# Optimization experiments

Measured on AMD Instinct MI355X. Metric: run time of the kernel, lower is better.

Reference implementation:

```python
import jax, jax.numpy as jnp
import numpy as np

N_SEARCH, B, C, H, W = 10, 32, 768, 24, 24
HT, WT = 8, 8
HEADS, POOL = 12, 4


def _G(t):
    # Integral of the bilinear triangle kernel: G(t) = int_{-1}^{t} max(0,1-|s|) ds
    tc = jnp.clip(t, -1.0, 1.0)
    return 0.5 + tc * (1.0 - 0.5 * jnp.abs(tc))


def prroi_pool(feats, rois, pool):
    # feats: [R,C,H,W], rois: [R,4] pixel coords (x0,y0,x1,y1); exact PrRoIPool2D
    R, C_, H_, W_ = feats.shape
    x0, y0, x1, y1 = rois[:, 0], rois[:, 1], rois[:, 2], rois[:, 3]
    bw = (x1 - x0) / pool
    bh = (y1 - y0) / pool
    p = jnp.arange(pool, dtype=feats.dtype)
    ex0 = x0[:, None] + p[None, :] * bw[:, None]   # [R,pool]
    ex1 = ex0 + bw[:, None]
    ey0 = y0[:, None] + p[None, :] * bh[:, None]
    ey1 = ey0 + bh[:, None]
    ix = jnp.arange(W_, dtype=feats.dtype)
    iy = jnp.arange(H_, dtype=feats.dtype)
    wx = _G(ex1[:, :, None] - ix) - _G(ex0[:, :, None] - ix)  # [R,pool,W]
    wy = _G(ey1[:, :, None] - iy) - _G(ey0[:, :, None] - iy)  # [R,pool,H]
    area = jnp.maximum(bw * bh, 1e-8)[:, None, None, None]
    return jnp.einsum('rph,rqw,rchw->rcpq', wy, wx, feats) / area  # [R,C,pool,pool]


def layernorm(x, g, b, eps=1e-5):
    m = jnp.mean(x, -1, keepdims=True)
    v = jnp.mean((x - m) ** 2, -1, keepdims=True)
    return (x - m) * jax.lax.rsqrt(v + eps) * g + b


def setup_inputs():
    key = jax.random.key(0)
    ks = jax.random.split(key, 24)
    search_feats = jax.random.normal(ks[0], (N_SEARCH, B, C, H, W), jnp.float32)
    template_feat = jax.random.normal(ks[1], (N_SEARCH, B, C, HT, WT), jnp.float32)
    u = jax.random.uniform(ks[2], (N_SEARCH, B, 4), jnp.float32)
    x0 = 0.05 + 0.4 * u[..., 0]
    y0 = 0.05 + 0.4 * u[..., 1]
    x1 = x0 + 0.15 + 0.3 * u[..., 2]
    y1 = y0 + 0.15 + 0.3 * u[..., 3]
    search_boxes = jnp.stack([x0, y0, x1, y1], -1)  # normalized, x1>x0, y1>y0
    s = 0.02
    d = {
        'search_feats': search_feats,
        'template_feat': template_feat,
        'search_boxes': search_boxes,
        'score_token': s * jax.random.normal(ks[3], (1, 1, C), jnp.float32),
        'ln1_g': jnp.ones((C,), jnp.float32), 'ln1_b': jnp.zeros((C,), jnp.float32),
        'Wq': s * jax.random.normal(ks[4], (2, C, C), jnp.float32), 'bq': jnp.zeros((2, C), jnp.float32),
        'Wk': s * jax.random.normal(ks[5], (2, C, C), jnp.float32), 'bk': jnp.zeros((2, C), jnp.float32),
        'Wv': s * jax.random.normal(ks[6], (2, C, C), jnp.float32), 'bv': jnp.zeros((2, C), jnp.float32),
        'Wo': s * jax.random.normal(ks[7], (2, C, C), jnp.float32), 'bo': jnp.zeros((2, C), jnp.float32),
        'ln2_g': jnp.ones((2, C), jnp.float32), 'ln2_b': jnp.zeros((2, C), jnp.float32),
        'Wmix': s * jax.random.normal(ks[8], (2, N_SEARCH, N_SEARCH), jnp.float32),
        'bmix': jnp.zeros((2, N_SEARCH), jnp.float32),
        'W1': s * jax.random.normal(ks[9], (C, C), jnp.float32), 'b1': jnp.zeros((C,), jnp.float32),
        'W2': s * jax.random.normal(ks[10], (C, C), jnp.float32), 'b2': jnp.zeros((C,), jnp.float32),
        'W3': s * jax.random.normal(ks[11], (C, 1), jnp.float32), 'b3': jnp.zeros((1,), jnp.float32),
    }
    return d


def reference(search_feats, template_feat, search_boxes, score_token, ln1_g, ln1_b,
              Wq, bq, Wk, bk, Wv, bv, Wo, bo, ln2_g, ln2_b, Wmix, bmix,
              W1, b1, W2, b2, W3, b3):
    N, b, c, h, w = search_feats.shape
    heads, pool = HEADS, POOL
    dh = c // heads
    scale = c ** (-0.5)  # note: full hidden_dim scale, as in original

    boxes = (search_boxes * w).reshape(-1, 4)              # [N*b,4] pixel coords
    feats = search_feats.reshape(-1, c, h, w)              # [N*b,c,h,w]
    pooled = prroi_pool(feats, boxes, pool)                # [N*b,c,pool,pool]
    # 'b c h w -> b (h w) c' then split N
    sbf = pooled.reshape(N, b, c, pool * pool).transpose(0, 1, 3, 2)  # [N,b,16,c]
    tmpl = template_feat.reshape(N, b, c, -1).transpose(0, 1, 3, 2)   # [N,b,64,c]

    x = jnp.broadcast_to(score_token, (N, b, 1, c))
    x = layernorm(x, ln1_g, ln1_b)
    kv = [sbf, tmpl]
    for i in range(2):
        q = x @ Wq[i] + bq[i]                              # [N,b,1,c]
        k = kv[i] @ Wk[i] + bk[i]                          # [N,b,T,c]
        v = kv[i] @ Wv[i] + bv[i]
        T = k.shape[2]
        qh = q.reshape(N, b, 1, heads, dh).transpose(0, 1, 3, 2, 4)   # [N,b,H,1,d]
        kh = k.reshape(N, b, T, heads, dh).transpose(0, 1, 3, 2, 4)   # [N,b,H,T,d]
        vh = v.reshape(N, b, T, heads, dh).transpose(0, 1, 3, 2, 4)
        attn = jax.nn.softmax(jnp.einsum('nbhld,nbhtd->nbhlt', qh, kh) * scale, -1)
        o = jnp.einsum('nbhlt,nbhtd->nbhld', attn, vh)
        o = o.transpose(0, 1, 3, 2, 4).reshape(N, b, 1, c)
        o = layernorm(o @ Wo[i] + bo[i], ln2_g[i], ln2_b[i])
        # time-mix across the N frames: [N,b,1,c] -> [b,c,N] -> linear -> [N,b,1,c]
        t = o[:, :, 0, :].transpose(1, 2, 0)               # [b,c,N]
        t = t @ Wmix[i] + bmix[i]
        x = t.transpose(2, 0, 1)[:, :, None, :]            # [N,b,1,c]

    hdd = jax.nn.relu(x @ W1 + b1)
    hdd = jax.nn.relu(hdd @ W2 + b2)
    return hdd @ W3 + b3                                   # [N,b,1,1]
```

## Files before the change

### kernel.cpp

```cpp
#include <hip/hip_runtime.h>
#include <cstdint>
#include <cstddef>

namespace {

constexpr float kScale = 0.03608439182435161f;
constexpr float kEps   = 1e-5f;

constexpr size_t OFF_QK0T = 0;
constexpr size_t OFF_QBK0 = 9216;
constexpr size_t OFF_S    = 16384;
constexpr size_t OFF_QK1  = OFF_S   + 2949120;
constexpr size_t OFF_O    = OFF_QK1 + 2949120;
constexpr size_t OFF_U    = OFF_O   + 245760;
constexpr size_t OFF_X    = OFF_U   + 245760;
constexpr size_t OFF_QF1  = OFF_X   + 245760;
constexpr size_t OFF_H1   = OFF_QF1 + 245760;
constexpr size_t OFF_H2   = OFF_H1  + 245760;
constexpr size_t OFF_WF   = OFF_H2  + 245760;

constexpr size_t WF_MAT_SHORTS = 1179648;

typedef short short8v __attribute__((ext_vector_type(8)));
typedef float float4v __attribute__((ext_vector_type(4)));

union BP  { int4 i4; short8v s8; };
union S4P { int2 i2; short s[4]; };

__device__ __forceinline__ void splitBf(float a, short &h, short &l){
    unsigned u = __float_as_uint(a);
    h = (short)(u >> 16);
    float r = a - __uint_as_float(u & 0xFFFF0000u);
    l = (short)(__float_as_uint(r) >> 16);
}

__device__ __forceinline__ float Gf(float t){
    float tc = fminf(fmaxf(t, -1.f), 1.f);
    return 0.5f + tc * (1.f - 0.5f * fabsf(tc));
}

__device__ __forceinline__ float blockReduce256(float v, float* red){
    #pragma unroll
    for (int off = 1; off < 64; off <<= 1) v += __shfl_xor(v, off);
    __syncthreads();
    if ((threadIdx.x & 63) == 0) red[threadIdx.x >> 6] = v;
    __syncthreads();
    return red[0] + red[1] + red[2] + red[3];
}

__global__ __launch_bounds__(256) void k_wprep(
        const float* __restrict__ w0, const float* __restrict__ w1,
        const float* __restrict__ w2, const float* __restrict__ w3,
        const float* __restrict__ w4, const float* __restrict__ w5,
        const float* __restrict__ w6, short* __restrict__ WF){
    const float* Wsel[7] = {w0,w1,w2,w3,w4,w5,w6};
    const float* W = Wsel[blockIdx.y];
    const int unit = blockIdx.x * 4 + (threadIdx.x >> 6);
    const int l = threadIdx.x & 63;
    const int kt = unit / 48, nb = unit % 48;
    const int n = nb*16 + (l & 15);
    const int kb = kt*32 + ((l >> 4) << 2);
    S4P hi0, hi1, lo0, lo1;
    #pragma unroll
    for (int e = 0; e < 4; ++e){
        float a = W[(size_t)(kb + e) * 768 + n];
        splitBf(a, hi0.s[e], lo0.s[e]);
        float b = W[(size_t)(kb + 16 + e) * 768 + n];
        splitBf(b, hi1.s[e], lo1.s[e]);
    }
    size_t base = (size_t)blockIdx.y * WF_MAT_SHORTS + (size_t)unit * 1024 + (size_t)l * 8;
    *(int2*)(WF + base)            = hi0.i2;
    *(int2*)(WF + base + 4)        = hi1.i2;
    *(int2*)(WF + base + 512)      = lo0.i2;
    *(int2*)(WF + base + 512 + 4)  = lo1.i2;
}

template<int HG, int RELU>
__global__ __launch_bounds__(256) void k_mgemm(
        const float* __restrict__ A, const short* __restrict__ WFm,
        const float* __restrict__ bias, float* __restrict__ C){
    __shared__ short AF[2][2][2][64][8];
    const int h   = blockIdx.y;
    const int m0  = blockIdx.x * 32;
    const int tid = threadIdx.x;
    const int l   = tid & 63;
    const int w   = tid >> 6;
    const int wm  = w >> 1, wn = w & 1;

    const int srow = tid >> 3, sk4 = tid & 7;
    const int sfm  = srow >> 4;
    const int slane = (srow & 15) + 16 * (sk4 & 3);
    const int sebase = 4 * (sk4 >> 2);
    const float* aRow = HG ? (A + ((size_t)(m0 + srow) * 12 + h) * 768)
                           : (A + (size_t)(m0 + srow) * 768);

    const int nb0 = h * 4 + wn * 2;
    const short* WB = WFm + (size_t)nb0 * 1024 + (size_t)l * 8;

    float4v acc0 = {0.f,0.f,0.f,0.f};
    float4v acc1 = {0.f,0.f,0.f,0.f};

    {
        float4 a0 = *(const float4*)(aRow + sk4 * 4);
        S4P hi, lo;
        splitBf(a0.x, hi.s[0], lo.s[0]); splitBf(a0.y, hi.s[1], lo.s[1]);
        splitBf(a0.z, hi.s[2], lo.s[2]); splitBf(a0.w, hi.s[3], lo.s[3]);
        *(int2*)&AF[0][sfm][0][slane][sebase] = hi.i2;
        *(int2*)&AF[0][sfm][1][slane][sebase] = lo.i2;
    }
    BP bh0, bl0, bh1, bl1;
    bh0.i4 = *(const int4*)(WB);
    bl0.i4 = *(const int4*)(WB + 512);
    bh1.i4 = *(const int4*)(WB + 1024);
    bl1.i4 = *(const int4*)(WB + 1536);
    __syncthreads();

    #pragma unroll 1
    for (int kt = 0; kt < 24; ++kt){
        const int cur = kt & 1;
        const int ktn = (kt < 23) ? kt + 1 : 23;
        float4 aN = *(const float4*)(aRow + ktn * 32 + sk4 * 4);
        BP cbh0 = bh0, cbl0 = bl0, cbh1 = bh1, cbl1 = bl1;
        {
            const short* wb = WB + (size_t)ktn * 49152;
            bh0.i4 = *(const int4*)(wb);
            bl0.i4 = *(const int4*)(wb + 512);
            bh1.i4 = *(const int4*)(wb + 1024);
            bl1.i4 = *(const int4*)(wb + 1536);
        }
        short8v ah = *(short8v*)&AF[cur][wm][0][l][0];
        short8v al = *(short8v*)&AF[cur][wm][1][l][0];
        acc0 = __builtin_amdgcn_mfma_f32_16x16x32_bf16(ah, cbh0.s8, acc0, 0, 0, 0);
        acc0 = __builtin_amdgcn_mfma_f32_16x16x32_bf16(al, cbh0.s8, acc0, 0, 0, 0);
        acc0 = __builtin_amdgcn_mfma_f32_16x16x32_bf16(ah, cbl0.s8, acc0, 0, 0, 0);
        acc1 = __builtin_amdgcn_mfma_f32_16x16x32_bf16(ah, cbh1.s8, acc1, 0, 0, 0);
        acc1 = __builtin_amdgcn_mfma_f32_16x16x32_bf16(al, cbh1.s8, acc1, 0, 0, 0);
        acc1 = __builtin_amdgcn_mfma_f32_16x16x32_bf16(ah, cbl1.s8, acc1, 0, 0, 0);
        if (kt < 23){
            S4P hi, lo;
            splitBf(aN.x, hi.s[0], lo.s[0]); splitBf(aN.y, hi.s[1], lo.s[1]);
            splitBf(aN.z, hi.s[2], lo.s[2]); splitBf(aN.w, hi.s[3], lo.s[3]);
            *(int2*)&AF[cur ^ 1][sfm][0][slane][sebase] = hi.i2;
            *(int2*)&AF[cur ^ 1][sfm][1][slane][sebase] = lo.i2;
        }
        __syncthreads();
    }

    const int col0 = h * 64 + (wn * 2 + 0) * 16 + (l & 15);
    const int col1 = h * 64 + (wn * 2 + 1) * 16 + (l & 15);
    const float b0 = bias[col0], b1 = bias[col1];
    #pragma unroll
    for (int reg = 0; reg < 4; ++reg){
        int row = m0 + wm * 16 + ((l >> 4) << 2) + reg;
        float v0 = acc0[reg] + b0;
        float v1 = acc1[reg] + b1;
        if (RELU){ v0 = fmaxf(v0, 0.f); v1 = fmaxf(v1, 0.f); }
        C[(size_t)row * 768 + col0] = v0;
        C[(size_t)row * 768 + col1] = v1;
    }
}

__global__ __launch_bounds__(256) void k_prep(
        const float* __restrict__ token, const float* __restrict__ g1,
        const float* __restrict__ b1,    const float* __restrict__ Wq0,
        const float* __restrict__ bq0,   const float* __restrict__ Wk0,
        const float* __restrict__ bk0,
        float* __restrict__ qk0T, float* __restrict__ qbk0){
    __shared__ float x0l[768];
    __shared__ float red[8];
    __shared__ float qfp[4][64];
    __shared__ float qfl[64];
    __shared__ float Ws[64][68];
    const int h  = blockIdx.x / 12;
    const int ct = blockIdx.x % 12;
    const int tid = threadIdx.x;

    float v0 = token[tid], v1 = token[tid+256], v2 = token[tid+512];
    float s = blockReduce256(v0+v1+v2, red);
    float m = s * (1.f/768.f);
    float d0 = v0-m, d1 = v1-m, d2 = v2-m;
    float qv = blockReduce256(d0*d0+d1*d1+d2*d2, red);
    float rs = rsqrtf(qv*(1.f/768.f) + kEps);
    x0l[tid]     = d0*rs*g1[tid]     + b1[tid];
    x0l[tid+256] = d1*rs*g1[tid+256] + b1[tid+256];
    x0l[tid+512] = d2*rs*g1[tid+512] + b1[tid+512];
    __syncthreads();

    {
        int dl = tid & 63, part = tid >> 6;
        int d = h*64 + dl;
        float a = 0.f;
        for (int c = part*192; c < part*192 + 192; ++c)
            a += x0l[c] * Wq0[(size_t)c*768 + d];
        qfp[part][dl] = a;
    }
    __syncthreads();
    if (tid < 64){
        int d = h*64 + tid;
        qfl[tid] = qfp[0][tid]+qfp[1][tid]+qfp[2][tid]+qfp[3][tid] + bq0[d];
    }
    __syncthreads();
    if (ct == 0 && tid < 64){
        float v = qfl[tid] * bk0[h*64 + tid];
        #pragma unroll
        for (int off = 1; off < 64; off <<= 1) v += __shfl_xor(v, off);
        if (tid == 0) qbk0[h] = v;
    }
    #pragma unroll
    for (int i = 0; i < 4; ++i){
        int f = tid + i*256; int cl = f >> 4, dd = (f & 15)*4;
        float4 v = *(const float4*)(Wk0 + (size_t)(ct*64+cl)*768 + h*64 + dd);
        *(float4*)&Ws[cl][dd] = v;
    }
    __syncthreads();
    {
        int cl = tid >> 2, part = tid & 3;
        float a = 0.f;
        #pragma unroll
        for (int jj = 0; jj < 16; ++jj){
            int dd = part*16 + jj;
            a += Ws[cl][dd] * qfl[dd];
        }
        a += __shfl_xor(a, 1); a += __shfl_xor(a, 2);
        if (part == 0) qk0T[h*768 + ct*64 + cl] = a;
    }
}

__global__ __launch_bounds__(256) void k_pool(
        const float* __restrict__ feats, const float* __restrict__ boxes,
        const float* __restrict__ qk0T,  const float* __restrict__ qbk0g,
        float* __restrict__ s0){
    __shared__ float P2[16][776];
    __shared__ float wxp[24][4];
    __shared__ float wyp[24][4];
    __shared__ float logitsL[12][17];
    __shared__ float attnT[16][12];
    __shared__ int   rng[4];
    __shared__ float areaInvS;
    const int r = blockIdx.x, tid = threadIdx.x;

    float bx0 = boxes[r*4+0]*24.f, by0 = boxes[r*4+1]*24.f;
    float bx1 = boxes[r*4+2]*24.f, by1 = boxes[r*4+3]*24.f;
    float bw = (bx1-bx0)*0.25f, bh = (by1-by0)*0.25f;
    if (tid == 0){
        int hlo = (int)floorf(by0) - 1; if (hlo < 0) hlo = 0;
        int hhi = (int)floorf(by1) + 1; if (hhi > 23) hhi = 23;
        int wlo = (int)floorf(bx0) - 1; if (wlo < 0) wlo = 0;
        int whi = (int)floorf(bx1) + 1; if (whi > 23) whi = 23;
        rng[0] = hlo; rng[1] = hhi; rng[2] = wlo >> 2; rng[3] = whi >> 2;
        areaInvS = 1.f / fmaxf(bw*bh, 1e-8f);
    }
    if (tid < 24){
        int w = tid;
        #pragma unroll
        for (int q = 0; q < 4; ++q){
            float e0 = bx0 + q*bw, e1 = e0 + bw;
            wxp[w][q] = Gf(e1 - (float)w) - Gf(e0 - (float)w);
        }
    } else if (tid < 48){
        int hh = tid - 24;
        #pragma unroll
        for (int p = 0; p < 4; ++p){
            float e0 = by0 + p*bh, e1 = e0 + bh;
            wyp[hh][p] = Gf(e1 - (float)hh) - Gf(e0 - (float)hh);
        }
    }
    __syncthreads();
    const int hlo = rng[0], hhi = rng[1], w4lo = rng[2], w4hi = rng[3];
    const float aInv = areaInvS;
    const int j = tid & 7;
    const int cbase = tid >> 3;

    for (int cg = 0; cg < 24; ++cg){
        int c = cg*32 + cbase;
        const float* fb = feats + ((size_t)r*768 + c)*576;
        float acc[16];
        #pragma unroll
        for (int k = 0; k < 16; ++k) acc[k] = 0.f;
        for (int hh = hlo + j; hh <= hhi; hh += 8){
            const float* rowp = fb + hh*24;
            float z[4] = {0.f,0.f,0.f,0.f};
            for (int w4 = w4lo; w4 <= w4hi; ++w4){
                float4 xv = *(const float4*)(rowp + w4*4);
                float xa[4] = {xv.x, xv.y, xv.z, xv.w};
                #pragma unroll
                for (int k = 0; k < 4; ++k){
                    float4 wv = *(const float4*)&wxp[w4*4+k][0];
                    z[0] += wv.x*xa[k]; z[1] += wv.y*xa[k];
                    z[2] += wv.z*xa[k]; z[3] += wv.w*xa[k];
                }
            }
            float4 wyv = *(const float4*)&wyp[hh][0];
            float wya[4] = {wyv.x, wyv.y, wyv.z, wyv.w};
            #pragma unroll
            for (int p = 0; p < 4; ++p)
                #pragma unroll
                for (int q = 0; q < 4; ++q)
                    acc[p*4+q] += wya[p]*z[q];
        }
        #pragma unroll
        for (int k = 0; k < 16; ++k){
            acc[k] += __shfl_xor(acc[k], 1);
            acc[k] += __shfl_xor(acc[k], 2);
            acc[k] += __shfl_xor(acc[k], 4);
        }
        P2[j][c]   = acc[j]   * aInv;
        P2[j+8][c] = acc[j+8] * aInv;
    }
    __syncthreads();

    if (tid < 192){
        int h = tid >> 4, t = tid & 15;
        float a = qbk0g[h];
        const float* qrow = qk0T + h*768;
        #pragma unroll 4
        for (int c4 = 0; c4 < 192; ++c4){
            float4 qv = *(const float4*)(qrow + c4*4);
            float4 pv = *(const float4*)&P2[t][c4*4];
            a += qv.x*pv.x + qv.y*pv.y + qv.z*pv.z + qv.w*pv.w;
        }
        logitsL[h][t] = a * kScale;
    }
    __syncthreads();
    if (tid < 12){
        float mx = -1e30f;
        for (int t = 0; t < 16; ++t) mx = fmaxf(mx, logitsL[tid][t]);
        float ss = 0.f;
        for (int t = 0; t < 16; ++t){
            float e = expf(logitsL[tid][t] - mx);
            attnT[t][tid] = e; ss += e;
        }
        float rsn = 1.f/ss;
        for (int t = 0; t < 16; ++t) attnT[t][tid] *= rsn;
    }
    __syncthreads();
    #pragma unroll
    for (int s3 = 0; s3 < 3; ++s3){
        int c = tid + s3*256;
        float a12[12];
        #pragma unroll
        for (int h = 0; h < 12; ++h) a12[h] = 0.f;
        #pragma unroll
        for (int t = 0; t < 16; ++t){
            float x = P2[t][c];
            float4 a0 = *(const float4*)&attnT[t][0];
            float4 a1 = *(const float4*)&attnT[t][4];
            float4 a2 = *(const float4*)&attnT[t][8];
            a12[0] += a0.x*x; a12[1] += a0.y*x; a12[2]  += a0.z*x; a12[3]  += a0.w*x;
            a12[4] += a1.x*x; a12[5] += a1.y*x; a12[6]  += a1.z*x; a12[7]  += a1.w*x;
            a12[8] += a2.x*x; a12[9] += a2.y*x; a12[10] += a2.z*x; a12[11] += a2.w*x;
        }
        #pragma unroll
        for (int h = 0; h < 12; ++h)
            s0[((size_t)r*12 + h)*768 + c] = a12[h];
    }
}

__global__ __launch_bounds__(256) void k_qk1(
        const float* __restrict__ qf1, const float* __restrict__ Wk1,
        float* __restrict__ qk1){
    __shared__ float As[32][68];
    __shared__ float Bs[64][68];
    const int r0 = blockIdx.x * 32, h = blockIdx.y, c0 = blockIdx.z * 64;
    const int tid = threadIdx.x;
    #pragma unroll
    for (int i = 0; i < 2; ++i){
        int f = tid + i*256; int ml = f >> 4, kk = (f & 15)*4;
        *(float4*)&As[ml][kk] =
            *(const float4*)(qf1 + (size_t)(r0+ml)*768 + h*64 + kk);
    }
    #pragma unroll
    for (int i = 0; i < 4; ++i){
        int f = tid + i*256; int cl = f >> 4, dd = (f & 15)*4;
        float4 v = *(const float4*)(Wk1 + (size_t)(c0+cl)*768 + h*64 + dd);
        Bs[dd+0][cl] = v.x; Bs[dd+1][cl] = v.y;
        Bs[dd+2][cl] = v.z; Bs[dd+3][cl] = v.w;
    }
    __syncthreads();
    const int tn = tid & 15, tm = tid >> 4;
    float acc0[4] = {0.f,0.f,0.f,0.f};
    float acc1[4] = {0.f,0.f,0.f,0.f};
    #pragma unroll
    for (int k4 = 0; k4 < 16; ++k4){
        float4 av0 = *(const float4*)&As[tm*2+0][k4*4];
        float4 av1 = *(const float4*)&As[tm*2+1][k4*4];
        float a0a[4] = {av0.x, av0.y, av0.z, av0.w};
        float a1a[4] = {av1.x, av1.y, av1.z, av1.w};
        #pragma unroll
        for (int jj = 0; jj < 4; ++jj){
            float4 bv = *(const float4*)&Bs[k4*4+jj][tn*4];
            acc0[0] += a0a[jj]*bv.x; acc0[1] += a0a[jj]*bv.y;
            acc0[2] += a0a[jj]*bv.z; acc0[3] += a0a[jj]*bv.w;
            acc1[0] += a1a[jj]*bv.x; acc1[1] += a1a[jj]*bv.y;
            acc1[2] += a1a[jj]*bv.z; acc1[3] += a1a[jj]*bv.w;
        }
    }
    float4 o0; o0.x=acc0[0]; o0.y=acc0[1]; o0.z=acc0[2]; o0.w=acc0[3];
    float4 o1; o1.x=acc1[0]; o1.y=acc1[1]; o1.z=acc1[2]; o1.w=acc1[3];
    *(float4*)(qk1 + ((size_t)(r0+tm*2+0)*12 + h)*768 + c0 + tn*4) = o0;
    *(float4*)(qk1 + ((size_t)(r0+tm*2+1)*12 + h)*768 + c0 + tn*4) = o1;
}

__global__ __launch_bounds__(256) void k_attn1(
        const float* __restrict__ tmpl, const float* __restrict__ qf1,
        const float* __restrict__ bk1,  const float* __restrict__ qk1,
        float* __restrict__ s1){
    __shared__ float Tc[192][68];
    __shared__ float logitsT[64][13];
    __shared__ float attnH[12][64];
    __shared__ float qbk[12];
    const int r = blockIdx.x, tid = threadIdx.x;
    const float* tp = tmpl + (size_t)r*768*64;

    if (tid < 192){
        int h = tid >> 4, pp = tid & 15;
        float v = 0.f;
        #pragma unroll
        for (int jj = 0; jj < 4; ++jj){
            int d = h*64 + pp*4 + jj;
            v += bk1[d] * qf1[(size_t)r*768 + d];
        }
        v += __shfl_xor(v,1); v += __shfl_xor(v,2);
        v += __shfl_xor(v,4); v += __shfl_xor(v,8);
        if (pp == 0) qbk[h] = v;
    }
    __syncthreads();
    float lacc[3];
    #pragma unroll
    for (int s = 0; s < 3; ++s){
        int task = tid + s*256;
        lacc[s] = qbk[task >> 6];
    }
    for (int cb = 0; cb < 4; ++cb){
        #pragma unroll
        for (int i = 0; i < 12; ++i){
            int f = tid + i*256; int cl = f >> 4, t4 = (f & 15)*4;
            *(float4*)&Tc[cl][t4] =
                *(const float4*)(tp + (size_t)(cb*192 + cl)*64 + t4);
        }
        __syncthreads();
        #pragma unroll
        for (int s = 0; s < 3; ++s){
            int task = tid + s*256;
            int h = task >> 6, t = task & 63;
            const float* qrow = qk1 + ((size_t)r*12 + h)*768 + cb*192;
            float a = 0.f;
            #pragma unroll 4
            for (int c4 = 0; c4 < 48; ++c4){
                float4 qv = *(const float4*)(qrow + c4*4);
                a += qv.x*Tc[c4*4+0][t] + qv.y*Tc[c4*4+1][t]
                   + qv.z*Tc[c4*4+2][t] + qv.w*Tc[c4*4+3][t];
            }
            lacc[s] += a;
        }
        __syncthreads();
    }
    #pragma unroll
    for (int s = 0; s < 3; ++s){
        int task = tid + s*256;
        logitsT[task & 63][task >> 6] = lacc[s] * kScale;
    }
    __syncthreads();
    if (tid < 12){
        float mx = -1e30f;
        for (int t = 0; t < 64; ++t) mx = fmaxf(mx, logitsT[t][tid]);
        float ss = 0.f;
        for (int t = 0; t < 64; ++t){
            float e = expf(logitsT[t][tid] - mx);
            attnH[tid][t] = e; ss += e;
        }
        float rsn = 1.f/ss;
        for (int t = 0; t < 64; ++t) attnH[tid][t] *= rsn;
    }
    __syncthreads();
    for (int cb = 0; cb < 4; ++cb){
        #pragma unroll
        for (int i = 0; i < 12; ++i){
            int f = tid + i*256; int cl = f >> 4, t4 = (f & 15)*4;
            *(float4*)&Tc[cl][t4] =
                *(const float4*)(tp + (size_t)(cb*192 + cl)*64 + t4);
        }
        __syncthreads();
        if (tid < 192){
            float4 trow[16];
            #pragma unroll
            for (int t4 = 0; t4 < 16; ++t4)
                trow[t4] = *(const float4*)&Tc[tid][t4*4];
            int c = cb*192 + tid;
            #pragma unroll
            for (int h = 0; h < 12; ++h){
                float a = 0.f;
                #pragma unroll
                for (int t4 = 0; t4 < 16; ++t4){
                    float4 avv = *(const float4*)&attnH[h][t4*4];
                    float4 tv = trow[t4];
                    a += avv.x*tv.x + avv.y*tv.y + avv.z*tv.z + avv.w*tv.w;
                }
                s1[((size_t)r*12 + h)*768 + c] = a;
            }
        }
        __syncthreads();
    }
}

__global__ __launch_bounds__(256) void k_lnmix(
        const float* __restrict__ u, const float* __restrict__ g,
        const float* __restrict__ bta, const float* __restrict__ Wmix,
        const float* __restrict__ bmix, float* __restrict__ xout){
    __shared__ float lnl[10][768];
    __shared__ float red[8];
    __shared__ float wm[100];
    __shared__ float bm[10];
    const int b = blockIdx.x, tid = threadIdx.x;
    if (tid < 100) wm[tid] = Wmix[tid];
    if (tid < 10)  bm[tid] = bmix[tid];
    for (int n = 0; n < 10; ++n){
        const float* row = u + (size_t)(n*32 + b)*768;
        float v0 = row[tid], v1 = row[tid+256], v2 = row[tid+512];
        float s = blockReduce256(v0+v1+v2, red);
        float m = s * (1.f/768.f);
        float d0 = v0-m, d1 = v1-m, d2 = v2-m;
        float qv = blockReduce256(d0*d0+d1*d1+d2*d2, red);
        float rs = rsqrtf(qv*(1.f/768.f) + kEps);
        lnl[n][tid]     = d0*rs*g[tid]     + bta[tid];
        lnl[n][tid+256] = d1*rs*g[tid+256] + bta[tid+256];
        lnl[n][tid+512] = d2*rs*g[tid+512] + bta[tid+512];
    }
    __syncthreads();
    #pragma unroll
    for (int s3 = 0; s3 < 3; ++s3){
        int c = tid + s3*256;
        float col[10];
        #pragma unroll
        for (int n = 0; n < 10; ++n) col[n] = lnl[n][c];
        #pragma unroll
        for (int np = 0; np < 10; ++np){
            float a = bm[np];
            #pragma unroll
            for (int n = 0; n < 10; ++n) a += col[n]*wm[n*10+np];
            xout[(size_t)(np*32 + b)*768 + c] = a;
        }
    }
}

__global__ __launch_bounds__(256) void k_head(
        const float* __restrict__ h2v, const float* __restrict__ W3,
        const float* __restrict__ b3, float* __restrict__ out){
    __shared__ float red[8];
    const int r = blockIdx.x, tid = threadIdx.x;
    const float* row = h2v + (size_t)r*768;
    float a = row[tid]*W3[tid] + row[tid+256]*W3[tid+256] + row[tid+512]*W3[tid+512];
    a = blockReduce256(a, red);
    if (tid == 0) out[r] = a + b3[0];
}

}

extern "C" void kernel_launch(void* const* d_in, const int* in_sizes, int n_in,
                              void* d_out, int out_size, void* d_ws, size_t ws_size,
                              hipStream_t stream){
    const float* feats = (const float*)d_in[0];
    const float* tmpl  = (const float*)d_in[1];
    const float* boxes = (const float*)d_in[2];
    const float* token = (const float*)d_in[3];
    const float* ln1g  = (const float*)d_in[4];
    const float* ln1b  = (const float*)d_in[5];
    const float* Wq    = (const float*)d_in[6];
    const float* bq    = (const float*)d_in[7];
    const float* Wk    = (const float*)d_in[8];
    const float* bk    = (const float*)d_in[9];
    const float* Wv    = (const float*)d_in[10];
    const float* bv    = (const float*)d_in[11];
    const float* Wo    = (const float*)d_in[12];
    const float* bo    = (const float*)d_in[13];
    const float* ln2g  = (const float*)d_in[14];
    const float* ln2b  = (const float*)d_in[15];
    const float* Wmix  = (const float*)d_in[16];
    const float* bmix  = (const float*)d_in[17];
    const float* W1    = (const float*)d_in[18];
    const float* b1v   = (const float*)d_in[19];
    const float* W2    = (const float*)d_in[20];
    const float* b2v   = (const float*)d_in[21];
    const float* W3    = (const float*)d_in[22];
    const float* b3v   = (const float*)d_in[23];
    float* ws  = (float*)d_ws;
    float* out = (float*)d_out;

    float* qk0T = ws + OFF_QK0T;
    float* qbk0 = ws + OFF_QBK0;
    float* sbuf = ws + OFF_S;
    float* qk1  = ws + OFF_QK1;
    float* obuf = ws + OFF_O;
    float* ubuf = ws + OFF_U;
    float* xbuf = ws + OFF_X;
    float* qf1  = ws + OFF_QF1;
    float* h1b  = ws + OFF_H1;
    float* h2b  = ws + OFF_H2;
    short* wf   = (short*)(ws + OFF_WF);

    const size_t MO = 589824;
    short* wfv0 = wf + 0*WF_MAT_SHORTS;
    short* wfo0 = wf + 1*WF_MAT_SHORTS;
    short* wfq1 = wf + 2*WF_MAT_SHORTS;
    short* wfv1 = wf + 3*WF_MAT_SHORTS;
    short* wfo1 = wf + 4*WF_MAT_SHORTS;
    short* wf1  = wf + 5*WF_MAT_SHORTS;
    short* wf2  = wf + 6*WF_MAT_SHORTS;

    k_wprep<<<dim3(288,7), 256, 0, stream>>>(Wv, Wo, Wq + MO, Wv + MO, Wo + MO, W1, W2, wf);
    k_prep<<<144, 256, 0, stream>>>(token, ln1g, ln1b, Wq, bq, Wk, bk, qk0T, qbk0);
    k_pool<<<320, 256, 0, stream>>>(feats, boxes, qk0T, qbk0, sbuf);
    k_mgemm<1,0><<<dim3(10,12), 256, 0, stream>>>(sbuf, wfv0, bv, obuf);
    k_mgemm<0,0><<<dim3(10,12), 256, 0, stream>>>(obuf, wfo0, bo, ubuf);
    k_lnmix<<<32, 256, 0, stream>>>(ubuf, ln2g, ln2b, Wmix, bmix, xbuf);
    k_mgemm<0,0><<<dim3(10,12), 256, 0, stream>>>(xbuf, wfq1, bq + 768, qf1);
    k_qk1<<<dim3(10,12,12), 256, 0, stream>>>(qf1, Wk + MO, qk1);
    k_attn1<<<320, 256, 0, stream>>>(tmpl, qf1, bk + 768, qk1, sbuf);
    k_mgemm<1,0><<<dim3(10,12), 256, 0, stream>>>(sbuf, wfv1, bv + 768, obuf);
    k_mgemm<0,0><<<dim3(10,12), 256, 0, stream>>>(obuf, wfo1, bo + 768, ubuf);
    k_lnmix<<<32, 256, 0, stream>>>(ubuf, ln2g + 768, ln2b + 768, Wmix + 100, bmix + 10, xbuf);
    k_mgemm<0,1><<<dim3(10,12), 256, 0, stream>>>(xbuf, wf1, b1v, h1b);
    k_mgemm<0,1><<<dim3(10,12), 256, 0, stream>>>(h1b, wf2, b2v, h2b);
    k_head<<<320, 256, 0, stream>>>(h2b, W3, b3v, out);
}
```

Baseline: 424.6 us.

## Split pooling across channel blocks and halve GEMM row tile for more blocks

```diff
diff --git a/kernel.cpp b/kernel.cpp
--- a/kernel.cpp
+++ b/kernel.cpp
@@ -18,8 +18,8 @@
 constexpr size_t OFF_H1   = OFF_QF1 + 245760;
 constexpr size_t OFF_H2   = OFF_H1  + 245760;
 constexpr size_t OFF_WF   = OFF_H2  + 245760;
-
 constexpr size_t WF_MAT_SHORTS = 1179648;
+constexpr size_t OFF_P    = OFF_WF + (7*WF_MAT_SHORTS)/2;
 
 typedef short short8v __attribute__((ext_vector_type(8)));
 typedef float float4v __attribute__((ext_vector_type(4)));
@@ -79,84 +79,72 @@
 __global__ __launch_bounds__(256) void k_mgemm(
         const float* __restrict__ A, const short* __restrict__ WFm,
         const float* __restrict__ bias, float* __restrict__ C){
-    __shared__ short AF[2][2][2][64][8];
+    __shared__ short AF[2][2][64][8];
     const int h   = blockIdx.y;
-    const int m0  = blockIdx.x * 32;
+    const int m0  = blockIdx.x * 16;
     const int tid = threadIdx.x;
     const int l   = tid & 63;
     const int w   = tid >> 6;
-    const int wm  = w >> 1, wn = w & 1;
 
     const int srow = tid >> 3, sk4 = tid & 7;
-    const int sfm  = srow >> 4;
-    const int slane = (srow & 15) + 16 * (sk4 & 3);
+    const int slane = srow + 16 * (sk4 & 3);
     const int sebase = 4 * (sk4 >> 2);
     const float* aRow = HG ? (A + ((size_t)(m0 + srow) * 12 + h) * 768)
                            : (A + (size_t)(m0 + srow) * 768);
 
-    const int nb0 = h * 4 + wn * 2;
-    const short* WB = WFm + (size_t)nb0 * 1024 + (size_t)l * 8;
-
-    float4v acc0 = {0.f,0.f,0.f,0.f};
-    float4v acc1 = {0.f,0.f,0.f,0.f};
-
-    {
+    const int nb = h * 4 + w;
+    const short* WB = WFm + (size_t)nb * 1024 + (size_t)l * 8;
+
+    float4v acc = {0.f,0.f,0.f,0.f};
+
+    if (tid < 128){
         float4 a0 = *(const float4*)(aRow + sk4 * 4);
         S4P hi, lo;
         splitBf(a0.x, hi.s[0], lo.s[0]); splitBf(a0.y, hi.s[1], lo.s[1]);
         splitBf(a0.z, hi.s[2], lo.s[2]); splitBf(a0.w, hi.s[3], lo.s[3]);
-        *(int2*)&AF[0][sfm][0][slane][sebase] = hi.i2;
-        *(int2*)&AF[0][sfm][1][slane][sebase] = lo.i2;
-    }
-    BP bh0, bl0, bh1, bl1;
-    bh0.i4 = *(const int4*)(WB);
-    bl0.i4 = *(const int4*)(WB + 512);
-    bh1.i4 = *(const int4*)(WB + 1024);
-    bl1.i4 = *(const int4*)(WB + 1536);
+        *(int2*)&AF[0][0][slane][sebase] = hi.i2;
+        *(int2*)&AF[0][1][slane][sebase] = lo.i2;
+    }
+    BP bh, bl;
+    bh.i4 = *(const int4*)(WB);
+    bl.i4 = *(const int4*)(WB + 512);
     __syncthreads();
 
     #pragma unroll 1
     for (int kt = 0; kt < 24; ++kt){
         const int cur = kt & 1;
         const int ktn = (kt < 23) ? kt + 1 : 23;
-        float4 aN = *(const float4*)(aRow + ktn * 32 + sk4 * 4);
-        BP cbh0 = bh0, cbl0 = bl0, cbh1 = bh1, cbl1 = bl1;
+        float4 aN;
+        if (tid < 128) aN = *(const float4*)(aRow + ktn * 32 + sk4 * 4);
+        BP cbh = bh, cbl = bl;
         {
             const short* wb = WB + (size_t)ktn * 49152;
-            bh0.i4 = *(const int4*)(wb);
-            bl0.i4 = *(const int4*)(wb + 512);
-            bh1.i4 = *(const int4*)(wb + 1024);
-            bl1.i4 = *(const int4*)(wb + 1536);
-        }
-        short8v ah = *(short8v*)&AF[cur][wm][0][l][0];
-        short8v al = *(short8v*)&AF[cur][wm][1][l][0];
-        acc0 = __builtin_amdgcn_mfma_f32_16x16x32_bf16(ah, cbh0.s8, acc0, 0, 0, 0);
-        acc0 = __builtin_amdgcn_mfma_f32_16x16x32_bf16(al, cbh0.s8, acc0, 0, 0, 0);
-        acc0 = __builtin_amdgcn_mfma_f32_16x16x32_bf16(ah, cbl0.s8, acc0, 0, 0, 0);
-        acc1 = __builtin_amdgcn_mfma_f32_16x16x32_bf16(ah, cbh1.s8, acc1, 0, 0, 0);
-        acc1 = __builtin_amdgcn_mfma_f32_16x16x32_bf16(al, cbh1.s8, acc1, 0, 0, 0);
-        acc1 = __builtin_amdgcn_mfma_f32_16x16x32_bf16(ah, cbl1.s8, acc1, 0, 0, 0);
-        if (kt < 23){
+            bh.i4 = *(const int4*)(wb);
+            bl.i4 = *(const int4*)(wb + 512);
+        }
+        short8v ah = *(short8v*)&AF[cur][0][l][0];
+        short8v al = *(short8v*)&AF[cur][1][l][0];
+        acc = __builtin_amdgcn_mfma_f32_16x16x32_bf16(ah, cbh.s8, acc, 0, 0, 0);
+        acc = __builtin_amdgcn_mfma_f32_16x16x32_bf16(al, cbh.s8, acc, 0, 0, 0);
+        acc = __builtin_amdgcn_mfma_f32_16x16x32_bf16(ah, cbl.s8, acc, 0, 0, 0);
+        if (kt < 23 && tid < 128){
             S4P hi, lo;
             splitBf(aN.x, hi.s[0], lo.s[0]); splitBf(aN.y, hi.s[1], lo.s[1]);
             splitBf(aN.z, hi.s[2], lo.s[2]); splitBf(aN.w, hi.s[3], lo.s[3]);
-            *(int2*)&AF[cur ^ 1][sfm][0][slane][sebase] = hi.i2;
-            *(int2*)&AF[cur ^ 1][sfm][1][slane][sebase] = lo.i2;
+            *(int2*)&AF[cur ^ 1][0][slane][sebase] = hi.i2;
+            *(int2*)&AF[cur ^ 1][1][slane][sebase] = lo.i2;
         }
         __syncthreads();
     }
 
-    const int col0 = h * 64 + (wn * 2 + 0) * 16 + (l & 15);
-    const int col1 = h * 64 + (wn * 2 + 1) * 16 + (l & 15);
-    const float b0 = bias[col0], b1 = bias[col1];
+    const int col = h * 64 + w * 16 + (l & 15);
+    const float bb = bias[col];
     #pragma unroll
     for (int reg = 0; reg < 4; ++reg){
-        int row = m0 + wm * 16 + ((l >> 4) << 2) + reg;
-        float v0 = acc0[reg] + b0;
-        float v1 = acc1[reg] + b1;
-        if (RELU){ v0 = fmaxf(v0, 0.f); v1 = fmaxf(v1, 0.f); }
-        C[(size_t)row * 768 + col0] = v0;
-        C[(size_t)row * 768 + col1] = v1;
+        int row = m0 + ((l >> 4) << 2) + reg;
+        float v = acc[reg] + bb;
+        if (RELU) v = fmaxf(v, 0.f);
+        C[(size_t)row * 768 + col] = v;
     }
 }
 
@@ -226,18 +214,15 @@
     }
 }
 
-__global__ __launch_bounds__(256) void k_pool(
+__global__ __launch_bounds__(256) void k_pool2(
         const float* __restrict__ feats, const float* __restrict__ boxes,
-        const float* __restrict__ qk0T,  const float* __restrict__ qbk0g,
-        float* __restrict__ s0){
-    __shared__ float P2[16][776];
+        float* __restrict__ P){
+    __shared__ float Xs[32*580];
     __shared__ float wxp[24][4];
     __shared__ float wyp[24][4];
-    __shared__ float logitsL[12][17];
-    __shared__ float attnT[16][12];
-    __shared__ int   rng[4];
+    __shared__ int   rng[2];
     __shared__ float areaInvS;
-    const int r = blockIdx.x, tid = threadIdx.x;
+    const int r = blockIdx.x, cc = blockIdx.y * 32, tid = threadIdx.x;
 
     float bx0 = boxes[r*4+0]*24.f, by0 = boxes[r*4+1]*24.f;
     float bx1 = boxes[r*4+2]*24.f, by1 = boxes[r*4+3]*24.f;
@@ -245,9 +230,7 @@
     if (tid == 0){
         int hlo = (int)floorf(by0) - 1; if (hlo < 0) hlo = 0;
         int hhi = (int)floorf(by1) + 1; if (hhi > 23) hhi = 23;
-        int wlo = (int)floorf(bx0) - 1; if (wlo < 0) wlo = 0;
-        int whi = (int)floorf(bx1) + 1; if (whi > 23) whi = 23;
-        rng[0] = hlo; rng[1] = hhi; rng[2] = wlo >> 2; rng[3] = whi >> 2;
+        rng[0] = hlo; rng[1] = hhi - hlo + 1;
         areaInvS = 1.f / fmaxf(bw*bh, 1e-8f);
     }
     if (tid < 24){
@@ -266,46 +249,77 @@
         }
     }
     __syncthreads();
-    const int hlo = rng[0], hhi = rng[1], w4lo = rng[2], w4hi = rng[3];
+    const int hlo = rng[0], nr = rng[1];
     const float aInv = areaInvS;
+
+    const int nf4 = nr * 192;
+    for (int idx = tid; idx < nf4; idx += 256){
+        int ri  = idx / 192;
+        int rem = idx - ri * 192;
+        int cl  = rem / 6;
+        int w4  = rem - cl * 6;
+        float4 v = *(const float4*)(feats + ((size_t)(r*768 + cc + cl))*576
+                                    + (hlo + ri)*24 + w4*4);
+        *(float4*)&Xs[cl*580 + ri*24 + w4*4] = v;
+    }
+    __syncthreads();
+
     const int j = tid & 7;
-    const int cbase = tid >> 3;
-
-    for (int cg = 0; cg < 24; ++cg){
-        int c = cg*32 + cbase;
-        const float* fb = feats + ((size_t)r*768 + c)*576;
-        float acc[16];
-        #pragma unroll
-        for (int k = 0; k < 16; ++k) acc[k] = 0.f;
-        for (int hh = hlo + j; hh <= hhi; hh += 8){
-            const float* rowp = fb + hh*24;
-            float z[4] = {0.f,0.f,0.f,0.f};
-            for (int w4 = w4lo; w4 <= w4hi; ++w4){
-                float4 xv = *(const float4*)(rowp + w4*4);
-                float xa[4] = {xv.x, xv.y, xv.z, xv.w};
-                #pragma unroll
-                for (int k = 0; k < 4; ++k){
-                    float4 wv = *(const float4*)&wxp[w4*4+k][0];
-                    z[0] += wv.x*xa[k]; z[1] += wv.y*xa[k];
-                    z[2] += wv.z*xa[k]; z[3] += wv.w*xa[k];
-                }
+    const int cl = tid >> 3;
+    float acc[16];
+    #pragma unroll
+    for (int k = 0; k < 16; ++k) acc[k] = 0.f;
+    for (int ri = j; ri < nr; ri += 8){
+        const float* xr = &Xs[cl*580 + ri*24];
+        float z[4] = {0.f,0.f,0.f,0.f};
+        #pragma unroll
+        for (int w4 = 0; w4 < 6; ++w4){
+            float4 xv = *(const float4*)(xr + w4*4);
+            float xa[4] = {xv.x, xv.y, xv.z, xv.w};
+            #pragma unroll
+            for (int k = 0; k < 4; ++k){
+                float4 wv = *(const float4*)&wxp[w4*4+k][0];
+                z[0] += wv.x*xa[k]; z[1] += wv.y*xa[k];
+                z[2] += wv.z*xa[k]; z[3] += wv.w*xa[k];
             }
-            float4 wyv = *(const float4*)&wyp[hh][0];
-            float wya[4] = {wyv.x, wyv.y, wyv.z, wyv.w};
+        }
+        float4 wyv = *(const float4*)&wyp[hlo+ri][0];
+        float wya[4] = {wyv.x, wyv.y, wyv.z, wyv.w};
+        #pragma unroll
+        for (int p = 0; p < 4; ++p)
             #pragma unroll
-            for (int p = 0; p < 4; ++p)
-                #pragma unroll
-                for (int q = 0; q < 4; ++q)
-                    acc[p*4+q] += wya[p]*z[q];
-        }
-        #pragma unroll
-        for (int k = 0; k < 16; ++k){
-            acc[k] += __shfl_xor(acc[k], 1);
-            acc[k] += __shfl_xor(acc[k], 2);
-            acc[k] += __shfl_xor(acc[k], 4);
-        }
-        P2[j][c]   = acc[j]   * aInv;
-        P2[j+8][c] = acc[j+8] * aInv;
+            for (int q = 0; q < 4; ++q)
+                acc[p*4+q] += wya[p]*z[q];
+    }
+    #pragma unroll
+    for (int k = 0; k < 16; ++k){
+        acc[k] += __shfl_xor(acc[k], 1);
+        acc[k] += __shfl_xor(acc[k], 2);
+        acc[k] += __shfl_xor(acc[k], 4);
+    }
+    float o0 = acc[0], o1 = acc[8];
+    #pragma unroll
+    for (int k = 1; k < 8; ++k){
+        if (j == k){ o0 = acc[k]; o1 = acc[k+8]; }
+    }
+    P[((size_t)r*16 + j)*768 + cc + cl]     = o0 * aInv;
+    P[((size_t)r*16 + j + 8)*768 + cc + cl] = o1 * aInv;
+}
+
+__global__ __launch_bounds__(256) void k_attn0(
+        const float* __restrict__ P, const float* __restrict__ qk0T,
+        const float* __restrict__ qbk0g, float* __restrict__ s0){
+    __shared__ float P2[16][776];
+    __shared__ float logitsL[12][17];
+    __shared__ float attnT[16][12];
+    const int r = blockIdx.x, tid = threadIdx.x;
+
+    #pragma unroll
+    for (int i = 0; i < 12; ++i){
+        int f = tid + i*256;
+        int t = f / 192, c4 = f - t*192;
+        float4 v = *(const float4*)(P + ((size_t)r*16 + t)*768 + c4*4);
+        *(float4*)&P2[t][c4*4] = v;
     }
     __syncthreads();
 
@@ -597,6 +611,7 @@
     float* h1b  = ws + OFF_H1;
     float* h2b  = ws + OFF_H2;
     short* wf   = (short*)(ws + OFF_WF);
+    float* Pbuf = ws + OFF_P;
 
     const size_t MO = 589824;
     short* wfv0 = wf + 0*WF_MAT_SHORTS;
@@ -609,17 +624,18 @@
 
     k_wprep<<<dim3(288,7), 256, 0, stream>>>(Wv, Wo, Wq + MO, Wv + MO, Wo + MO, W1, W2, wf);
     k_prep<<<144, 256, 0, stream>>>(token, ln1g, ln1b, Wq, bq, Wk, bk, qk0T, qbk0);
-    k_pool<<<320, 256, 0, stream>>>(feats, boxes, qk0T, qbk0, sbuf);
-    k_mgemm<1,0><<<dim3(10,12), 256, 0, stream>>>(sbuf, wfv0, bv, obuf);
-    k_mgemm<0,0><<<dim3(10,12), 256, 0, stream>>>(obuf, wfo0, bo, ubuf);
+    k_pool2<<<dim3(320,24), 256, 0, stream>>>(feats, boxes, Pbuf);
+    k_attn0<<<320, 256, 0, stream>>>(Pbuf, qk0T, qbk0, sbuf);
+    k_mgemm<1,0><<<dim3(20,12), 256, 0, stream>>>(sbuf, wfv0, bv, obuf);
+    k_mgemm<0,0><<<dim3(20,12), 256, 0, stream>>>(obuf, wfo0, bo, ubuf);
     k_lnmix<<<32, 256, 0, stream>>>(ubuf, ln2g, ln2b, Wmix, bmix, xbuf);
-    k_mgemm<0,0><<<dim3(10,12), 256, 0, stream>>>(xbuf, wfq1, bq + 768, qf1);
+    k_mgemm<0,0><<<dim3(20,12), 256, 0, stream>>>(xbuf, wfq1, bq + 768, qf1);
     k_qk1<<<dim3(10,12,12), 256, 0, stream>>>(qf1, Wk + MO, qk1);
     k_attn1<<<320, 256, 0, stream>>>(tmpl, qf1, bk + 768, qk1, sbuf);
-    k_mgemm<1,0><<<dim3(10,12), 256, 0, stream>>>(sbuf, wfv1, bv + 768, obuf);
-    k_mgemm<0,0><<<dim3(10,12), 256, 0, stream>>>(obuf, wfo1, bo + 768, ubuf);
+    k_mgemm<1,0><<<dim3(20,12), 256, 0, stream>>>(sbuf, wfv1, bv + 768, obuf);
+    k_mgemm<0,0><<<dim3(20,12), 256, 0, stream>>>(obuf, wfo1, bo + 768, ubuf);
     k_lnmix<<<32, 256, 0, stream>>>(ubuf, ln2g + 768, ln2b + 768, Wmix + 100, bmix + 10, xbuf);
-    k_mgemm<0,1><<<dim3(10,12), 256, 0, stream>>>(xbuf, wf1, b1v, h1b);
-    k_mgemm<0,1><<<dim3(10,12), 256, 0, stream>>>(h1b, wf2, b2v, h2b);
+    k_mgemm<0,1><<<dim3(20,12), 256, 0, stream>>>(xbuf, wf1, b1v, h1b);
+    k_mgemm<0,1><<<dim3(20,12), 256, 0, stream>>>(h1b, wf2, b2v, h2b);
     k_head<<<320, 256, 0, stream>>>(h2b, W3, b3v, out);
 }
```

After: 404.3 us. -4.8%, faster.
